# Kernel tuning notes

Hardware: AMD Instinct MI355X
Metric: run time of the kernel (lower is better)

The kernel has to match this reference:

```python
import jax, jax.numpy as jnp
import numpy as np

N = 100000   # nodes
E = 800000   # edges
D = 64       # feature dim (input=hidden=output)
EPS = 1e-5   # BatchNorm eps


def setup_inputs() -> dict:
    key = jax.random.key(0)
    ks = jax.random.split(key, 24)
    s = 1.0 / np.sqrt(D)
    inp = {
        "x": jax.random.normal(ks[0], (N, D), jnp.float32),
        "edge_index": jax.random.randint(ks[1], (2, E), 0, N, jnp.int64),
        # GCNConv weights (x @ W + b after normalized aggregation)
        "W1": jax.random.normal(ks[2], (D, D), jnp.float32) * s,
        "b1": jax.random.normal(ks[3], (D,), jnp.float32) * 0.01,
        "W2": jax.random.normal(ks[4], (D, D), jnp.float32) * s,
        "b2": jax.random.normal(ks[5], (D,), jnp.float32) * 0.01,
        "W3": jax.random.normal(ks[6], (D, D), jnp.float32) * s,
        "b3": jax.random.normal(ks[7], (D,), jnp.float32) * 0.01,
        # BatchNorm1d (inference: running stats)
        "bn1_g": jax.random.uniform(ks[8], (D,), jnp.float32, 0.5, 1.5),
        "bn1_b": jax.random.normal(ks[9], (D,), jnp.float32) * 0.1,
        "bn1_m": jax.random.normal(ks[10], (D,), jnp.float32) * 0.1,
        "bn1_v": jax.random.uniform(ks[11], (D,), jnp.float32, 0.5, 1.5),
        "bn2_g": jax.random.uniform(ks[12], (D,), jnp.float32, 0.5, 1.5),
        "bn2_b": jax.random.normal(ks[13], (D,), jnp.float32) * 0.1,
        "bn2_m": jax.random.normal(ks[14], (D,), jnp.float32) * 0.1,
        "bn2_v": jax.random.uniform(ks[15], (D,), jnp.float32, 0.5, 1.5),
        # predictor MLP: Linear -> tanh -> (dropout=id) -> Linear
        "pW1": jax.random.normal(ks[16], (D, D), jnp.float32) * s,
        "pb1": jax.random.normal(ks[17], (D,), jnp.float32) * 0.01,
        "pW2": jax.random.normal(ks[18], (D, D), jnp.float32) * s,
        "pb2": jax.random.normal(ks[19], (D,), jnp.float32) * 0.01,
    }
    return inp


def _gcn_norm(edge_index):
    # add self loops, compute sym-normalized edge coefficients (PyG GCNConv)
    loop = jnp.arange(N, dtype=edge_index.dtype)
    src = jnp.concatenate([edge_index[0], loop])
    dst = jnp.concatenate([edge_index[1], loop])
    deg = jax.ops.segment_sum(jnp.ones(src.shape[0], jnp.float32), dst, num_segments=N)
    dis = jax.lax.rsqrt(deg)  # deg >= 1 due to self loops
    norm = dis[src] * dis[dst]
    return src, dst, norm


def _gcn_layer(x, src, dst, norm, W, b):
    h = x @ W                              # [N, D] small GEMM
    msg = h[src] * norm[:, None]           # [E+N, D] gather (memory bound)
    return jax.ops.segment_sum(msg, dst, num_segments=N) + b  # scatter-add


def _bn(x, g, b, m, v):
    return (x - m) * (g * jax.lax.rsqrt(v + EPS)) + b


def reference(x, edge_index, W1, b1, W2, b2, W3, b3,
              bn1_g, bn1_b, bn1_m, bn1_v, bn2_g, bn2_b, bn2_m, bn2_v,
              pW1, pb1, pW2, pb2):
    src, dst, norm = _gcn_norm(edge_index)
    h = _gcn_layer(x, src, dst, norm, W1, b1)
    h = jax.nn.relu(_bn(h, bn1_g, bn1_b, bn1_m, bn1_v))   # dropout = id (eval)
    h = _gcn_layer(h, src, dst, norm, W2, b2)
    h = jax.nn.relu(_bn(h, bn2_g, bn2_b, bn2_m, bn2_v))
    h = _gcn_layer(h, src, dst, norm, W3, b3)
    out = jnp.tanh(h @ pW1 + pb1) @ pW2 + pb2              # predictor MLP
    return out
```

## Files before the change

### kernel.cpp

```cpp
#include <hip/hip_runtime.h>
#include <hip/hip_fp16.h>

#define N_NODES 100000
#define N_EDGES 800000
#define DIM 64
#define BN_EPS 1e-5f
#define LDX 68
#define EDGE_CAP 1600000

__global__ __launch_bounds__(256) void k_cvt_count(const float* __restrict__ x,
                                                   __half* __restrict__ xh,
                                                   const int* __restrict__ dst,
                                                   int* __restrict__ deg,
                                                   int* __restrict__ rank) {
    int idx = blockIdx.x * blockDim.x + threadIdx.x;
    if (idx < 1600000) {
        float4 v = ((const float4*)x)[idx];
        unsigned int u0 = __half_as_ushort(__float2half(v.x));
        unsigned int u1 = __half_as_ushort(__float2half(v.y));
        unsigned int u2 = __half_as_ushort(__float2half(v.z));
        unsigned int u3 = __half_as_ushort(__float2half(v.w));
        ((uint2*)xh)[idx] = make_uint2(u0 | (u1 << 16), u2 | (u3 << 16));
    }
    if (idx < N_EDGES) rank[idx] = atomicAdd(&deg[dst[idx]], 1);
}

__global__ __launch_bounds__(256) void k_scan_fuse(const int* __restrict__ deg,
                                                   int* __restrict__ row_off,
                                                   float* __restrict__ dinv,
                                                   int* __restrict__ gcount,
                                                   const float* __restrict__ W3,
                                                   const float* __restrict__ b3,
                                                   const float* __restrict__ pW1,
                                                   const float* __restrict__ pb1,
                                                   float* __restrict__ W3p,
                                                   float* __restrict__ b3p) {
    int tid = threadIdx.x;
    if (blockIdx.x == 98) {
        int c = tid & 63;
        int kbase = (tid >> 6) * 16;
        for (int k = kbase; k < kbase + 16; ++k) {
            float acc = 0.f;
#pragma unroll 8
            for (int j = 0; j < 64; ++j)
                acc = fmaf(W3[k * 64 + j], pW1[j * 64 + c], acc);
            W3p[k * 64 + c] = acc;
        }
        if (tid < 64) {
            float acc = pb1[c];
#pragma unroll 8
            for (int j = 0; j < 64; ++j)
                acc = fmaf(b3[j], pW1[j * 64 + c], acc);
            b3p[c] = acc;
        }
        return;
    }
    __shared__ int sdata[256];
    __shared__ int sbase;
    int base = blockIdx.x * 1024 + tid * 4;
    int4 d = make_int4(0, 0, 0, 0);
    int4 v = make_int4(0, 0, 0, 0);
    if (base < N_NODES) {
        d = *(const int4*)(deg + base);
        v.x = (d.x + 7) & ~7;
        v.y = (d.y + 7) & ~7;
        v.z = (d.z + 7) & ~7;
        v.w = (d.w + 7) & ~7;
    }
    int tsum = v.x + v.y + v.z + v.w;
    sdata[tid] = tsum;
    __syncthreads();
    for (int off = 1; off < 256; off <<= 1) {
        int t = (tid >= off) ? sdata[tid - off] : 0;
        __syncthreads();
        sdata[tid] += t;
        __syncthreads();
    }
    if (tid == 255) sbase = atomicAdd(gcount, sdata[255]);
    __syncthreads();
    if (base >= N_NODES) return;
    int excl = sdata[tid] - tsum + sbase;
    int4 o;
    o.x = excl;
    o.y = o.x + v.x;
    o.z = o.y + v.y;
    o.w = o.z + v.z;
    *(int4*)(row_off + base) = o;
    float4 di;
    di.x = rsqrtf((float)(d.x + 1));
    di.y = rsqrtf((float)(d.y + 1));
    di.z = rsqrtf((float)(d.z + 1));
    di.w = rsqrtf((float)(d.w + 1));
    *(float4*)(dinv + base) = di;
}

__global__ __launch_bounds__(256) void k_build(const int* __restrict__ ei,
                                               const int* __restrict__ rank,
                                               const int* __restrict__ row_off,
                                               int* __restrict__ esrc) {
    int idx = blockIdx.x * 256 + threadIdx.x;
    if (idx >= 200000) return;
    int4 s4 = ((const int4*)ei)[idx];
    int4 d4 = ((const int4*)(ei + N_EDGES))[idx];
    int4 r4 = ((const int4*)rank)[idx];
    esrc[row_off[d4.x] + r4.x] = s4.x;
    esrc[row_off[d4.y] + r4.y] = s4.y;
    esrc[row_off[d4.z] + r4.z] = s4.z;
    esrc[row_off[d4.w] + r4.w] = s4.w;
}

__global__ __launch_bounds__(256) void k_aggregate(const __half* __restrict__ xin,
                                                   const int* __restrict__ row_off,
                                                   const int* __restrict__ deg,
                                                   const int* __restrict__ esrc,
                                                   const float* __restrict__ dinv,
                                                   __half* __restrict__ out) {
    int lane16 = threadIdx.x & 15;
    int node = blockIdx.x * 16 + (threadIdx.x >> 4);
    float di = dinv[node];
    int beg = row_off[node];
    int len = deg[node];

    uint2 us = ((const uint2*)(xin + (size_t)node * DIM))[lane16];
    float w0 = di * di;
    float4 acc;
    acc.x = __half2float(__ushort_as_half((unsigned short)(us.x & 0xffff))) * w0;
    acc.y = __half2float(__ushort_as_half((unsigned short)(us.x >> 16))) * w0;
    acc.z = __half2float(__ushort_as_half((unsigned short)(us.y & 0xffff))) * w0;
    acc.w = __half2float(__ushort_as_half((unsigned short)(us.y >> 16))) * w0;

    int lenmax = len;
    lenmax = max(lenmax, __shfl_xor(lenmax, 16, 64));
    lenmax = max(lenmax, __shfl_xor(lenmax, 32, 64));

    int lclamp = (len > 0) ? (len - 1) : 0;
    for (int i = 0; i < lenmax; i += 8) {
#pragma unroll
        for (int u = 0; u < 8; ++u) {
            int j = i + u;
            int jc = j < lclamp ? j : lclamp;
            int s = esrc[beg + jc];
            s = ((unsigned)s < N_NODES) ? s : 0;
            float w = (j < len) ? dinv[s] * di : 0.f;
            uint2 u2 = ((const uint2*)(xin + (size_t)s * DIM))[lane16];
            acc.x = fmaf(w, __half2float(__ushort_as_half((unsigned short)(u2.x & 0xffff))), acc.x);
            acc.y = fmaf(w, __half2float(__ushort_as_half((unsigned short)(u2.x >> 16))), acc.y);
            acc.z = fmaf(w, __half2float(__ushort_as_half((unsigned short)(u2.y & 0xffff))), acc.z);
            acc.w = fmaf(w, __half2float(__ushort_as_half((unsigned short)(u2.y >> 16))), acc.w);
        }
    }

    unsigned int p0 = __half_as_ushort(__float2half(acc.x)) |
                      (__half_as_ushort(__float2half(acc.y)) << 16);
    unsigned int p1 = __half_as_ushort(__float2half(acc.z)) |
                      (__half_as_ushort(__float2half(acc.w)) << 16);
    ((uint2*)(out + (size_t)node * DIM))[lane16] = make_uint2(p0, p1);
}

#define GEMM_STEP(SX, SW)                                                      \
    {                                                                          \
        float4 a0 = *(const float4*)&SX[(r0 + 0) * LDX + k4 * 4];              \
        float4 a1 = *(const float4*)&SX[(r0 + 1) * LDX + k4 * 4];              \
        float4 a2 = *(const float4*)&SX[(r0 + 2) * LDX + k4 * 4];              \
        float4 a3 = *(const float4*)&SX[(r0 + 3) * LDX + k4 * 4];              \
        float4 b0 = *(const float4*)&SW[(k4 * 4 + 0) * 64 + c0];               \
        float4 b1 = *(const float4*)&SW[(k4 * 4 + 1) * 64 + c0];               \
        float4 b2 = *(const float4*)&SW[(k4 * 4 + 2) * 64 + c0];               \
        float4 b3 = *(const float4*)&SW[(k4 * 4 + 3) * 64 + c0];               \
        const float* ap[4] = {&a0.x, &a1.x, &a2.x, &a3.x};                     \
        _Pragma("unroll") for (int i = 0; i < 4; ++i) {                        \
            float x0 = ap[i][0], x1 = ap[i][1], x2 = ap[i][2], x3 = ap[i][3];  \
            acc[i][0] = fmaf(x0, b0.x, acc[i][0]);                             \
            acc[i][1] = fmaf(x0, b0.y, acc[i][1]);                             \
            acc[i][2] = fmaf(x0, b0.z, acc[i][2]);                             \
            acc[i][3] = fmaf(x0, b0.w, acc[i][3]);                             \
            acc[i][0] = fmaf(x1, b1.x, acc[i][0]);                             \
            acc[i][1] = fmaf(x1, b1.y, acc[i][1]);                             \
            acc[i][2] = fmaf(x1, b1.z, acc[i][2]);                             \
            acc[i][3] = fmaf(x1, b1.w, acc[i][3]);                             \
            acc[i][0] = fmaf(x2, b2.x, acc[i][0]);                             \
            acc[i][1] = fmaf(x2, b2.y, acc[i][1]);                             \
            acc[i][2] = fmaf(x2, b2.z, acc[i][2]);                             \
            acc[i][3] = fmaf(x2, b2.w, acc[i][3]);                             \
            acc[i][0] = fmaf(x3, b3.x, acc[i][0]);                             \
            acc[i][1] = fmaf(x3, b3.y, acc[i][1]);                             \
            acc[i][2] = fmaf(x3, b3.z, acc[i][2]);                             \
            acc[i][3] = fmaf(x3, b3.w, acc[i][3]);                             \
        }                                                                      \
    }

#define STAGE_H2F(SRCPTR, SXPTR)                                               \
    {                                                                          \
        int r = tid >> 2;                                                      \
        int q = tid & 3;                                                       \
        int row = row0 + r;                                                    \
        float4* dst = (float4*)(SXPTR + r * LDX);                              \
        if (row < N_NODES) {                                                   \
            const uint2* src = (const uint2*)(SRCPTR + (size_t)row * DIM);     \
            _Pragma("unroll") for (int m = 0; m < 4; ++m) {                    \
                uint2 u = src[q + m * 4];                                      \
                float4 f;                                                      \
                f.x = __half2float(__ushort_as_half((unsigned short)(u.x & 0xffff)));       \
                f.y = __half2float(__ushort_as_half((unsigned short)(u.x >> 16)));          \
                f.z = __half2float(__ushort_as_half((unsigned short)(u.y & 0xffff)));       \
                f.w = __half2float(__ushort_as_half((unsigned short)(u.y >> 16)));          \
                dst[q + m * 4] = f;                                            \
            }                                                                  \
        } else {                                                               \
            float4 z = make_float4(0.f, 0.f, 0.f, 0.f);                        \
            _Pragma("unroll") for (int m = 0; m < 4; ++m) dst[q + m * 4] = z;  \
        }                                                                      \
    }

__global__ __launch_bounds__(256) void k_gemm_bn_h(const __half* __restrict__ xin,
                                                   const float* __restrict__ W,
                                                   const float* __restrict__ bias,
                                                   const float* __restrict__ bng,
                                                   const float* __restrict__ bnb,
                                                   const float* __restrict__ bnm,
                                                   const float* __restrict__ bnv,
                                                   __half* __restrict__ out) {
    __shared__ float sW[4096];
    __shared__ float sX[64 * LDX];
    int tid = threadIdx.x;
    int row0 = blockIdx.x * 64;

    for (int i = tid; i < 1024; i += 256)
        ((float4*)sW)[i] = ((const float4*)W)[i];
    STAGE_H2F(xin, sX)
    __syncthreads();

    int cq = tid & 15, rq = tid >> 4;
    int c0 = cq * 4, r0 = rq * 4;
    float acc[4][4];
#pragma unroll
    for (int i = 0; i < 4; ++i)
#pragma unroll
        for (int j = 0; j < 4; ++j) acc[i][j] = 0.f;

#pragma unroll 4
    for (int k4 = 0; k4 < 16; ++k4) GEMM_STEP(sX, sW)

    float4 bv = *(const float4*)&bias[c0];
    float4 g = *(const float4*)&bng[c0];
    float4 bb = *(const float4*)&bnb[c0];
    float4 m = *(const float4*)&bnm[c0];
    float4 vv = *(const float4*)&bnv[c0];
    float A0 = g.x * rsqrtf(vv.x + BN_EPS);
    float A1 = g.y * rsqrtf(vv.y + BN_EPS);
    float A2 = g.z * rsqrtf(vv.z + BN_EPS);
    float A3 = g.w * rsqrtf(vv.w + BN_EPS);
    float B0 = (bv.x - m.x) * A0 + bb.x;
    float B1 = (bv.y - m.y) * A1 + bb.y;
    float B2 = (bv.z - m.z) * A2 + bb.z;
    float B3 = (bv.w - m.w) * A3 + bb.w;
#pragma unroll
    for (int i = 0; i < 4; ++i) {
        int row = row0 + r0 + i;
        if (row >= N_NODES) break;
        unsigned int u0 = __half_as_ushort(__float2half(fmaxf(0.f, fmaf(acc[i][0], A0, B0))));
        unsigned int u1 = __half_as_ushort(__float2half(fmaxf(0.f, fmaf(acc[i][1], A1, B1))));
        unsigned int u2 = __half_as_ushort(__float2half(fmaxf(0.f, fmaf(acc[i][2], A2, B2))));
        unsigned int u3 = __half_as_ushort(__float2half(fmaxf(0.f, fmaf(acc[i][3], A3, B3))));
        *(uint2*)(out + (size_t)row * DIM + c0) = make_uint2(u0 | (u1 << 16), u2 | (u3 << 16));
    }
}

__global__ __launch_bounds__(256) void k_tail(const __half* __restrict__ xin,
                                              const float* __restrict__ W3p,
                                              const float* __restrict__ b3p,
                                              const float* __restrict__ pW2,
                                              const float* __restrict__ pb2,
                                              float* __restrict__ out) {
    __shared__ float sW1[4096];
    __shared__ float sW2[4096];
    __shared__ float sX[64 * LDX];
    int tid = threadIdx.x;
    int row0 = blockIdx.x * 64;

    for (int i = tid; i < 1024; i += 256) {
        ((float4*)sW1)[i] = ((const float4*)W3p)[i];
        ((float4*)sW2)[i] = ((const float4*)pW2)[i];
    }
    STAGE_H2F(xin, sX)
    __syncthreads();

    int cq = tid & 15, rq = tid >> 4;
    int c0 = cq * 4, r0 = rq * 4;
    float acc[4][4];

#pragma unroll
    for (int i = 0; i < 4; ++i)
#pragma unroll
        for (int j = 0; j < 4; ++j) acc[i][j] = 0.f;
#pragma unroll 4
    for (int k4 = 0; k4 < 16; ++k4) GEMM_STEP(sX, sW1)
    __syncthreads();

    {
        float4 bv = *(const float4*)&b3p[c0];
#pragma unroll
        for (int i = 0; i < 4; ++i) {
            float4 h;
            h.x = tanhf(acc[i][0] + bv.x);
            h.y = tanhf(acc[i][1] + bv.y);
            h.z = tanhf(acc[i][2] + bv.z);
            h.w = tanhf(acc[i][3] + bv.w);
            *(float4*)&sX[(r0 + i) * LDX + c0] = h;
        }
    }
    __syncthreads();

#pragma unroll
    for (int i = 0; i < 4; ++i)
#pragma unroll
        for (int j = 0; j < 4; ++j) acc[i][j] = 0.f;
#pragma unroll 4
    for (int k4 = 0; k4 < 16; ++k4) GEMM_STEP(sX, sW2)

    float4 bv = *(const float4*)&pb2[c0];
#pragma unroll
    for (int i = 0; i < 4; ++i) {
        int row = row0 + r0 + i;
        if (row >= N_NODES) break;
        float4 o;
        o.x = acc[i][0] + bv.x;
        o.y = acc[i][1] + bv.y;
        o.z = acc[i][2] + bv.z;
        o.w = acc[i][3] + bv.w;
        *(float4*)(out + (size_t)row * DIM + c0) = o;
    }
}

extern "C" void kernel_launch(void* const* d_in, const int* in_sizes, int n_in,
                              void* d_out, int out_size, void* d_ws, size_t ws_size,
                              hipStream_t stream) {
    const float* x     = (const float*)d_in[0];
    const int*   ei    = (const int*)d_in[1];
    const float* W1    = (const float*)d_in[2];
    const float* b1    = (const float*)d_in[3];
    const float* W2    = (const float*)d_in[4];
    const float* b2    = (const float*)d_in[5];
    const float* W3    = (const float*)d_in[6];
    const float* b3    = (const float*)d_in[7];
    const float* bn1_g = (const float*)d_in[8];
    const float* bn1_b = (const float*)d_in[9];
    const float* bn1_m = (const float*)d_in[10];
    const float* bn1_v = (const float*)d_in[11];
    const float* bn2_g = (const float*)d_in[12];
    const float* bn2_b = (const float*)d_in[13];
    const float* bn2_m = (const float*)d_in[14];
    const float* bn2_v = (const float*)d_in[15];
    const float* pW1   = (const float*)d_in[16];
    const float* pb1   = (const float*)d_in[17];
    const float* pW2   = (const float*)d_in[18];
    const float* pb2   = (const float*)d_in[19];
    float* out = (float*)d_out;

    char* ws = (char*)d_ws;
    int*    deg     = (int*)ws;                      ws += 100352 * 4;
    int*    gcount  = (int*)ws;                      ws += 4 * 4;
    int*    row_off = (int*)ws;                      ws += 100352 * 4;
    int*    rank    = (int*)ws;                      ws += (size_t)N_EDGES * 4;
    int*    esrc    = (int*)ws;                      ws += (size_t)EDGE_CAP * 4;
    float*  dinv    = (float*)ws;                    ws += 100352 * 4;
    float*  W3p     = (float*)ws;                    ws += 4096 * 4;
    float*  b3p     = (float*)ws;                    ws += 64 * 4;
    __half* xh      = (__half*)ws;                   ws += (size_t)N_NODES * DIM * 2;
    __half* hbuf    = (__half*)ws;                   ws += (size_t)N_NODES * DIM * 2;
    __half* abuf    = (__half*)ws;                   ws += (size_t)N_NODES * DIM * 2;

    const int blk = 256;
    int gCvt   = 6250;
    int gBuild = 782;
    int gAgg   = N_NODES / 16;
    int gTile  = (N_NODES + 63) / 64;

    hipMemsetAsync(deg, 0, (size_t)(100352 + 4) * 4, stream);
    k_cvt_count<<<gCvt, blk, 0, stream>>>(x, xh, ei + N_EDGES, deg, rank);
    k_scan_fuse<<<99, blk, 0, stream>>>(deg, row_off, dinv, gcount,
                                        W3, b3, pW1, pb1, W3p, b3p);
    k_build<<<gBuild, blk, 0, stream>>>(ei, rank, row_off, esrc);

    k_aggregate<<<gAgg, blk, 0, stream>>>(xh, row_off, deg, esrc, dinv, abuf);
    k_gemm_bn_h<<<gTile, blk, 0, stream>>>(abuf, W1, b1, bn1_g, bn1_b, bn1_m, bn1_v, hbuf);

    k_aggregate<<<gAgg, blk, 0, stream>>>(hbuf, row_off, deg, esrc, dinv, abuf);
    k_gemm_bn_h<<<gTile, blk, 0, stream>>>(abuf, W2, b2, bn2_g, bn2_b, bn2_m, bn2_v, hbuf);

    k_aggregate<<<gAgg, blk, 0, stream>>>(hbuf, row_off, deg, esrc, dinv, abuf);
    k_tail<<<gTile, blk, 0, stream>>>(abuf, W3p, b3p, pW2, pb2, out);
}
```

Before: 380.5 us.

## Split fp16 feature buffers into 8 column planes and precompute edge weights

Feature buffers are stored as eight planes of 8 halves (16 bytes) per node, and aggregation runs one slice per block, with two threads per node per slice. The intent is that each plane (about 1.6 MB) fits in cache, so random gathers reuse cached lines instead of pulling whole 128-byte rows. The CSR build now stores (src, dinv[src]*dinv[dst]) pairs, which removes the per-edge dinv gather during aggregation but doubles the edge array size. The edge list is now read 8 times per layer, once per slice, and the loop uses per-thread variable trip counts with no unrolling, so wavefronts can diverge.

```diff
diff --git a/kernel.cpp b/kernel.cpp
--- a/kernel.cpp
+++ b/kernel.cpp
@@ -7,6 +7,9 @@
 #define BN_EPS 1e-5f
 #define LDX 68
 #define EDGE_CAP 1600000
+#define PROWS 100352
+#define PSTRB ((size_t)PROWS * 16)
+
 
 __global__ __launch_bounds__(256) void k_cvt_count(const float* __restrict__ x,
                                                    __half* __restrict__ xh,
@@ -20,7 +23,9 @@
         unsigned int u1 = __half_as_ushort(__float2half(v.y));
         unsigned int u2 = __half_as_ushort(__float2half(v.z));
         unsigned int u3 = __half_as_ushort(__float2half(v.w));
-        ((uint2*)xh)[idx] = make_uint2(u0 | (u1 << 16), u2 | (u3 << 16));
+        int row = idx >> 4, c = idx & 15;
+        *(uint2*)((char*)xh + (size_t)(c >> 1) * PSTRB + (size_t)row * 16 + (c & 1) * 8)
+            = make_uint2(u0 | (u1 << 16), u2 | (u3 << 16));
     }
     if (idx < N_EDGES) rank[idx] = atomicAdd(&deg[dst[idx]], 1);
 }
@@ -97,64 +102,58 @@
 __global__ __launch_bounds__(256) void k_build(const int* __restrict__ ei,
                                                const int* __restrict__ rank,
                                                const int* __restrict__ row_off,
-                                               int* __restrict__ esrc) {
+                                               const float* __restrict__ dinv,
+                                               int2* __restrict__ edges) {
     int idx = blockIdx.x * 256 + threadIdx.x;
     if (idx >= 200000) return;
     int4 s4 = ((const int4*)ei)[idx];
     int4 d4 = ((const int4*)(ei + N_EDGES))[idx];
     int4 r4 = ((const int4*)rank)[idx];
-    esrc[row_off[d4.x] + r4.x] = s4.x;
-    esrc[row_off[d4.y] + r4.y] = s4.y;
-    esrc[row_off[d4.z] + r4.z] = s4.z;
-    esrc[row_off[d4.w] + r4.w] = s4.w;
+    edges[row_off[d4.x] + r4.x] = make_int2(s4.x, __float_as_int(dinv[s4.x] * dinv[d4.x]));
+    edges[row_off[d4.y] + r4.y] = make_int2(s4.y, __float_as_int(dinv[s4.y] * dinv[d4.y]));
+    edges[row_off[d4.z] + r4.z] = make_int2(s4.z, __float_as_int(dinv[s4.z] * dinv[d4.z]));
+    edges[row_off[d4.w] + r4.w] = make_int2(s4.w, __float_as_int(dinv[s4.w] * dinv[d4.w]));
 }
 
 __global__ __launch_bounds__(256) void k_aggregate(const __half* __restrict__ xin,
                                                    const int* __restrict__ row_off,
                                                    const int* __restrict__ deg,
-                                                   const int* __restrict__ esrc,
+                                                   const int2* __restrict__ edges,
                                                    const float* __restrict__ dinv,
                                                    __half* __restrict__ out) {
-    int lane16 = threadIdx.x & 15;
-    int node = blockIdx.x * 16 + (threadIdx.x >> 4);
+    int slice = blockIdx.x & 7;
+    int node = (blockIdx.x >> 3) * 128 + (threadIdx.x >> 1);
+    if (node >= N_NODES) return;
+    int h8 = threadIdx.x & 1;
+    const char* plane = (const char*)xin + (size_t)slice * PSTRB;
+    char* oplane = (char*)out + (size_t)slice * PSTRB;
+
     float di = dinv[node];
-    int beg = row_off[node];
-    int len = deg[node];
-
-    uint2 us = ((const uint2*)(xin + (size_t)node * DIM))[lane16];
     float w0 = di * di;
+    uint2 us = *(const uint2*)(plane + (size_t)node * 16 + h8 * 8);
     float4 acc;
     acc.x = __half2float(__ushort_as_half((unsigned short)(us.x & 0xffff))) * w0;
     acc.y = __half2float(__ushort_as_half((unsigned short)(us.x >> 16))) * w0;
     acc.z = __half2float(__ushort_as_half((unsigned short)(us.y & 0xffff))) * w0;
     acc.w = __half2float(__ushort_as_half((unsigned short)(us.y >> 16))) * w0;
 
-    int lenmax = len;
-    lenmax = max(lenmax, __shfl_xor(lenmax, 16, 64));
-    lenmax = max(lenmax, __shfl_xor(lenmax, 32, 64));
-
-    int lclamp = (len > 0) ? (len - 1) : 0;
-    for (int i = 0; i < lenmax; i += 8) {
-#pragma unroll
-        for (int u = 0; u < 8; ++u) {
-            int j = i + u;
-            int jc = j < lclamp ? j : lclamp;
-            int s = esrc[beg + jc];
-            s = ((unsigned)s < N_NODES) ? s : 0;
-            float w = (j < len) ? dinv[s] * di : 0.f;
-            uint2 u2 = ((const uint2*)(xin + (size_t)s * DIM))[lane16];
-            acc.x = fmaf(w, __half2float(__ushort_as_half((unsigned short)(u2.x & 0xffff))), acc.x);
-            acc.y = fmaf(w, __half2float(__ushort_as_half((unsigned short)(u2.x >> 16))), acc.y);
-            acc.z = fmaf(w, __half2float(__ushort_as_half((unsigned short)(u2.y & 0xffff))), acc.z);
-            acc.w = fmaf(w, __half2float(__ushort_as_half((unsigned short)(u2.y >> 16))), acc.w);
-        }
+    int beg = row_off[node];
+    int len = deg[node];
+    for (int j = 0; j < len; ++j) {
+        int2 e = edges[beg + j];
+        float w = __int_as_float(e.y);
+        uint2 u2 = *(const uint2*)(plane + (size_t)e.x * 16 + h8 * 8);
+        acc.x = fmaf(w, __half2float(__ushort_as_half((unsigned short)(u2.x & 0xffff))), acc.x);
+        acc.y = fmaf(w, __half2float(__ushort_as_half((unsigned short)(u2.x >> 16))), acc.y);
+        acc.z = fmaf(w, __half2float(__ushort_as_half((unsigned short)(u2.y & 0xffff))), acc.z);
+        acc.w = fmaf(w, __half2float(__ushort_as_half((unsigned short)(u2.y >> 16))), acc.w);
     }
 
     unsigned int p0 = __half_as_ushort(__float2half(acc.x)) |
                       (__half_as_ushort(__float2half(acc.y)) << 16);
     unsigned int p1 = __half_as_ushort(__float2half(acc.z)) |
                       (__half_as_ushort(__float2half(acc.w)) << 16);
-    ((uint2*)(out + (size_t)node * DIM))[lane16] = make_uint2(p0, p1);
+    *(uint2*)(oplane + (size_t)node * 16 + h8 * 8) = make_uint2(p0, p1);
 }
 
 #define GEMM_STEP(SX, SW)                                                      \
@@ -189,22 +188,24 @@
         }                                                                      \
     }
 
-#define STAGE_H2F(SRCPTR, SXPTR)                                               \
+#define STAGE_H2F_S(SRCPTR, SXPTR)                                             \
     {                                                                          \
         int r = tid >> 2;                                                      \
         int q = tid & 3;                                                       \
         int row = row0 + r;                                                    \
         float4* dst = (float4*)(SXPTR + r * LDX);                              \
         if (row < N_NODES) {                                                   \
-            const uint2* src = (const uint2*)(SRCPTR + (size_t)row * DIM);     \
             _Pragma("unroll") for (int m = 0; m < 4; ++m) {                    \
-                uint2 u = src[q + m * 4];                                      \
+                int c = q + m * 4;                                             \
+                uint2 u = *(const uint2*)((const char*)(SRCPTR) +              \
+                          (size_t)(c >> 1) * PSTRB + (size_t)row * 16 +        \
+                          (c & 1) * 8);                                        \
                 float4 f;                                                      \
                 f.x = __half2float(__ushort_as_half((unsigned short)(u.x & 0xffff)));       \
                 f.y = __half2float(__ushort_as_half((unsigned short)(u.x >> 16)));          \
                 f.z = __half2float(__ushort_as_half((unsigned short)(u.y & 0xffff)));       \
                 f.w = __half2float(__ushort_as_half((unsigned short)(u.y >> 16)));          \
-                dst[q + m * 4] = f;                                            \
+                dst[c] = f;                                                    \
             }                                                                  \
         } else {                                                               \
             float4 z = make_float4(0.f, 0.f, 0.f, 0.f);                        \
@@ -227,7 +228,7 @@
 
     for (int i = tid; i < 1024; i += 256)
         ((float4*)sW)[i] = ((const float4*)W)[i];
-    STAGE_H2F(xin, sX)
+    STAGE_H2F_S(xin, sX)
     __syncthreads();
 
     int cq = tid & 15, rq = tid >> 4;
@@ -254,6 +255,7 @@
     float B1 = (bv.y - m.y) * A1 + bb.y;
     float B2 = (bv.z - m.z) * A2 + bb.z;
     float B3 = (bv.w - m.w) * A3 + bb.w;
+    char* oplane = (char*)out + (size_t)(cq >> 1) * PSTRB + (cq & 1) * 8;
 #pragma unroll
     for (int i = 0; i < 4; ++i) {
         int row = row0 + r0 + i;
@@ -262,7 +264,7 @@
         unsigned int u1 = __half_as_ushort(__float2half(fmaxf(0.f, fmaf(acc[i][1], A1, B1))));
         unsigned int u2 = __half_as_ushort(__float2half(fmaxf(0.f, fmaf(acc[i][2], A2, B2))));
         unsigned int u3 = __half_as_ushort(__float2half(fmaxf(0.f, fmaf(acc[i][3], A3, B3))));
-        *(uint2*)(out + (size_t)row * DIM + c0) = make_uint2(u0 | (u1 << 16), u2 | (u3 << 16));
+        *(uint2*)(oplane + (size_t)row * 16) = make_uint2(u0 | (u1 << 16), u2 | (u3 << 16));
     }
 }
 
@@ -282,7 +284,7 @@
         ((float4*)sW1)[i] = ((const float4*)W3p)[i];
         ((float4*)sW2)[i] = ((const float4*)pW2)[i];
     }
-    STAGE_H2F(xin, sX)
+    STAGE_H2F_S(xin, sX)
     __syncthreads();
 
     int cq = tid & 15, rq = tid >> 4;
@@ -362,32 +364,32 @@
     int*    gcount  = (int*)ws;                      ws += 4 * 4;
     int*    row_off = (int*)ws;                      ws += 100352 * 4;
     int*    rank    = (int*)ws;                      ws += (size_t)N_EDGES * 4;
-    int*    esrc    = (int*)ws;                      ws += (size_t)EDGE_CAP * 4;
+    int2*   edges   = (int2*)ws;                     ws += (size_t)EDGE_CAP * 8;
     float*  dinv    = (float*)ws;                    ws += 100352 * 4;
     float*  W3p     = (float*)ws;                    ws += 4096 * 4;
     float*  b3p     = (float*)ws;                    ws += 64 * 4;
-    __half* xh      = (__half*)ws;                   ws += (size_t)N_NODES * DIM * 2;
-    __half* hbuf    = (__half*)ws;                   ws += (size_t)N_NODES * DIM * 2;
-    __half* abuf    = (__half*)ws;                   ws += (size_t)N_NODES * DIM * 2;
+    __half* xh      = (__half*)ws;                   ws += 8 * PSTRB;
+    __half* hbuf    = (__half*)ws;                   ws += 8 * PSTRB;
+    __half* abuf    = (__half*)ws;                   ws += 8 * PSTRB;
 
     const int blk = 256;
     int gCvt   = 6250;
     int gBuild = 782;
-    int gAgg   = N_NODES / 16;
+    int gAgg   = 8 * 782;
     int gTile  = (N_NODES + 63) / 64;
 
     hipMemsetAsync(deg, 0, (size_t)(100352 + 4) * 4, stream);
     k_cvt_count<<<gCvt, blk, 0, stream>>>(x, xh, ei + N_EDGES, deg, rank);
     k_scan_fuse<<<99, blk, 0, stream>>>(deg, row_off, dinv, gcount,
                                         W3, b3, pW1, pb1, W3p, b3p);
-    k_build<<<gBuild, blk, 0, stream>>>(ei, rank, row_off, esrc);
-
-    k_aggregate<<<gAgg, blk, 0, stream>>>(xh, row_off, deg, esrc, dinv, abuf);
+    k_build<<<gBuild, blk, 0, stream>>>(ei, rank, row_off, dinv, edges);
+
+    k_aggregate<<<gAgg, blk, 0, stream>>>(xh, row_off, deg, edges, dinv, abuf);
     k_gemm_bn_h<<<gTile, blk, 0, stream>>>(abuf, W1, b1, bn1_g, bn1_b, bn1_m, bn1_v, hbuf);
 
-    k_aggregate<<<gAgg, blk, 0, stream>>>(hbuf, row_off, deg, esrc, dinv, abuf);
+    k_aggregate<<<gAgg, blk, 0, stream>>>(hbuf, row_off, deg, edges, dinv, abuf);
     k_gemm_bn_h<<<gTile, blk, 0, stream>>>(abuf, W2, b2, bn2_g, bn2_b, bn2_m, bn2_v, hbuf);
 
-    k_aggregate<<<gAgg, blk, 0, stream>>>(hbuf, row_off, deg, esrc, dinv, abuf);
+    k_aggregate<<<gAgg, blk, 0, stream>>>(hbuf, row_off, deg, edges, dinv, abuf);
     k_tail<<<gTile, blk, 0, stream>>>(abuf, W3p, b3p, pW2, pb2, out);
 }
```

New measurement: 454.2 us. 1.19x slower.
